# Kernel optimization log

Measured on AMD Instinct MI355X. Metric: run time of the kernel, lower is better.

## Reference

```python
import jax, jax.numpy as jnp
import numpy as np

ALPHA = 0.2  # LeakyReLU negative slope
NEG_BIG = -9e15


def setup_inputs() -> dict:
    key = jax.random.key(0)
    k1, k2, k3, k4 = jax.random.split(key, 4)
    N, F_in, F_out = 8192, 512, 256
    h = jax.random.normal(k1, (N, F_in), dtype=jnp.float32)
    adj = jax.random.randint(k2, (N, N), 0, 2, dtype=jnp.int32)
    # xavier_uniform with gain=1.414
    lim_W = 1.414 * np.sqrt(6.0 / (F_in + F_out))
    W = jax.random.uniform(k3, (F_in, F_out), jnp.float32, -lim_W, lim_W)
    lim_a = 1.414 * np.sqrt(6.0 / (2 * F_out + 1))
    a = jax.random.uniform(k4, (2 * F_out, 1), jnp.float32, -lim_a, lim_a)
    return {"h": h, "adj": adj, "W": W, "a": a}


def reference(h, adj, W, a):
    # Wh: [N, F_out]
    Wh = h @ W
    F_out = Wh.shape[1]
    # Decomposed score: e_ij = leakyrelu(a1.Wh_i + a2.Wh_j)
    f1 = Wh @ a[:F_out, 0]   # [N]
    f2 = Wh @ a[F_out:, 0]   # [N]
    e = f1[:, None] + f2[None, :]          # [N, N]
    e = jax.nn.leaky_relu(e, ALPHA)
    e = jnp.where(adj > 0, e, NEG_BIG)
    attention = jax.nn.softmax(e, axis=1)  # dropout omitted (eval mode)
    h_prime = attention @ Wh               # [N, F_out]
    return jax.nn.elu(h_prime)             # concat=True
```

## Files before the change

### kernel.cpp

```cpp
#include <hip/hip_runtime.h>
#include <hip/hip_bf16.h>
#include <cstdint>

#define NV 8192
#define FIN 512
#define FOUT 256
#define KS 4
#define ALPHA_LRELU 0.2f

using bf16x8 = __attribute__((ext_vector_type(8))) short;
using f32x4  = __attribute__((ext_vector_type(4))) float;

static __device__ __forceinline__ float b2f(ushort u) {
  union { uint32_t u32; float f; } v; v.u32 = ((uint32_t)u) << 16; return v.f;
}
static __device__ __forceinline__ ushort f2b(float f) {
  union { float f; uint32_t u; } v; v.f = f;
  uint32_t r = (v.u + 0x7fffu + ((v.u >> 16) & 1u)) >> 16;
  return (ushort)r;
}
static __device__ __forceinline__ int swz(int row, int kchunk) {
  return (row << 6) + (((kchunk ^ (row & 7)) & 7) << 3);
}
static __device__ __forceinline__ void gl_lds16(const ushort* g, ushort* l) {
  __builtin_amdgcn_global_load_lds(
      (const __attribute__((address_space(1))) uint32_t*)(uintptr_t)g,
      (__attribute__((address_space(3))) uint32_t*)(uint32_t)(uintptr_t)l,
      16, 0, 0);
}

__global__ void k_prep_h(const float* __restrict__ h, ushort* __restrict__ hB) {
  int idx = blockIdx.x * 256 + threadIdx.x;
  float4 v = ((const float4*)h)[idx];
  ushort4 o;
  o.x = f2b(v.x); o.y = f2b(v.y); o.z = f2b(v.z); o.w = f2b(v.w);
  ((ushort4*)hB)[idx] = o;
}

__global__ void k_prep_w(const float* __restrict__ W, ushort* __restrict__ WT) {
  int t = blockIdx.x * 256 + threadIdx.x;
  int n = t >> 9, k = t & 511;
  WT[(size_t)n * FIN + k] = f2b(W[(size_t)k * FOUT + n]);
}

__global__ __launch_bounds__(256, 4) void k_gemm1(
    const ushort* __restrict__ hB, const ushort* __restrict__ WT,
    ushort* __restrict__ WhT) {
  __shared__ __align__(16) ushort As[64 * 64];
  __shared__ __align__(16) ushort Ws[64 * 64];
  const int t = threadIdx.x;
  const int lane = t & 63;
  const int w = t >> 6;
  const int wm = w >> 1, wn = w & 1;
  const int i0 = blockIdx.x * 64;
  const int n0 = blockIdx.y * 64;

  f32x4 acc[2][2] = {};
  const int srow = t & 63, sseg = t >> 6;

  for (int kt = 0; kt < FIN / 64; ++kt) {
    const int k0 = kt * 64;
    const uint4* gA = (const uint4*)(hB + (size_t)(i0 + srow) * FIN + k0 + sseg * 16);
    const uint4* gB = (const uint4*)(WT + (size_t)(n0 + srow) * FIN + k0 + sseg * 16);
#pragma unroll
    for (int m = 0; m < 2; ++m) {
      uint4 va = gA[m];
      *(uint4*)&As[swz(srow, sseg * 2 + m)] = va;
      uint4 vb = gB[m];
      *(uint4*)&Ws[swz(srow, sseg * 2 + m)] = vb;
    }
    __syncthreads();
#pragma unroll
    for (int kk = 0; kk < 2; ++kk) {
      const int kc = kk * 4 + (lane >> 4);
      bf16x8 af[2], bfv[2];
#pragma unroll
      for (int fi = 0; fi < 2; ++fi)
        af[fi] = *(const bf16x8*)&As[swz(wm * 32 + fi * 16 + (lane & 15), kc)];
#pragma unroll
      for (int fj = 0; fj < 2; ++fj)
        bfv[fj] = *(const bf16x8*)&Ws[swz(wn * 32 + fj * 16 + (lane & 15), kc)];
#pragma unroll
      for (int fi = 0; fi < 2; ++fi)
#pragma unroll
        for (int fj = 0; fj < 2; ++fj)
          acc[fi][fj] = __builtin_amdgcn_mfma_f32_16x16x32_bf16(af[fi], bfv[fj], acc[fi][fj], 0, 0, 0);
    }
    __syncthreads();
  }
#pragma unroll
  for (int fi = 0; fi < 2; ++fi) {
    const int row0 = i0 + wm * 32 + fi * 16 + ((lane >> 4) << 2);
#pragma unroll
    for (int fj = 0; fj < 2; ++fj) {
      const int col = n0 + wn * 32 + fj * 16 + (lane & 15);
      ushort4 o;
      o.x = f2b(acc[fi][fj][0]); o.y = f2b(acc[fi][fj][1]);
      o.z = f2b(acc[fi][fj][2]); o.w = f2b(acc[fi][fj][3]);
      *(ushort4*)&WhT[(size_t)col * NV + row0] = o;
    }
  }
}

__global__ void k_f12(const ushort* __restrict__ WhT, const float* __restrict__ a,
                      float* __restrict__ f1, float* __restrict__ f2,
                      float* __restrict__ f2bmax) {
  __shared__ float a1s[256], a2s[256];
  __shared__ float r1[4][64], r2[4][64];
  const int tid = threadIdx.x;
  a1s[tid] = a[tid];
  a2s[tid] = a[256 + tid];
  const int ws = tid >> 6, ln = tid & 63;
  const int i = blockIdx.x * 64 + ln;
  __syncthreads();
  float s1 = 0.f, s2 = 0.f;
#pragma unroll 8
  for (int c = ws * 64; c < ws * 64 + 64; ++c) {
    float v = b2f(WhT[(size_t)c * NV + i]);
    s1 = fmaf(v, a1s[c], s1);
    s2 = fmaf(v, a2s[c], s2);
  }
  r1[ws][ln] = s1; r2[ws][ln] = s2;
  __syncthreads();
  if (ws == 0) {
    s1 = r1[0][ln] + r1[1][ln] + r1[2][ln] + r1[3][ln];
    s2 = r2[0][ln] + r2[1][ln] + r2[2][ln] + r2[3][ln];
    f1[i] = s1; f2[i] = s2;
    float m = s2;
#pragma unroll
    for (int off = 32; off > 0; off >>= 1) m = fmaxf(m, __shfl_xor(m, off));
    if (ln == 0) f2bmax[blockIdx.x] = m;
  }
}

__global__ void k_fmax(const float* __restrict__ f2bmax, float* __restrict__ mfp) {
  __shared__ float red[128];
  const int tid = threadIdx.x;
  red[tid] = f2bmax[tid];
  __syncthreads();
  for (int off = 64; off > 0; off >>= 1) {
    if (tid < off) red[tid] = fmaxf(red[tid], red[tid + off]);
    __syncthreads();
  }
  if (tid == 0) mfp[0] = red[0];
}

__global__ __launch_bounds__(512, 2) void k_gemm2(
    const int* __restrict__ adj, const ushort* __restrict__ WhT,
    const float* __restrict__ f1, const float* __restrict__ f2,
    const float* __restrict__ mfp,
    float* __restrict__ accP, float* __restrict__ Sp) {
  __shared__ __align__(16) ushort Ps[2][64 * 64];
  __shared__ __align__(16) ushort Bs[2][256 * 64];

  const int t = threadIdx.x;
  const int lane = t & 63;
  const int w = t >> 6;
  const int wm = w >> 2, wn = w & 3;
  const int bid = blockIdx.x;
  const int ks = bid & (KS - 1);
  const int rb = bid >> 2;
  const int i0 = rb * 64;
  const int jbase = ks * (NV / KS);
  const int NT = (NV / KS) / 64;

  const int pr = t >> 3, pq = t & 7;
  const float mf = mfp[0];
  const float f1r = f1[i0 + pr];
  const float e0 = f1r + mf;
  const float cr = fmaxf(e0, ALPHA_LRELU * e0);

  const int lrow = lane >> 3;
  const int lchunk = (lane & 7) ^ lrow;
  const ushort* wsrc0 = WhT + (size_t)(w * 32 + lrow) * NV + jbase + lchunk * 8;
  const int* adjp = adj + (size_t)(i0 + pr) * NV + jbase + pq * 8;
  const float* f2p = f2 + jbase + pq * 8;

  float ssum = 0.f;
  f32x4 acc[2][4] = {};
  int av[8]; float fz[8];

  auto stage_load = [&](int koff, int buf) {
#pragma unroll
    for (int q = 0; q < 4; ++q)
      gl_lds16(wsrc0 + (size_t)q * 8 * NV + koff, &Bs[buf][(w * 4 + q) * 512]);
    int4 a0 = *(const int4*)(adjp + koff);
    int4 a1 = *(const int4*)(adjp + koff + 4);
    float4 z0 = *(const float4*)(f2p + koff);
    float4 z1 = *(const float4*)(f2p + koff + 4);
    av[0] = a0.x; av[1] = a0.y; av[2] = a0.z; av[3] = a0.w;
    av[4] = a1.x; av[5] = a1.y; av[6] = a1.z; av[7] = a1.w;
    fz[0] = z0.x; fz[1] = z0.y; fz[2] = z0.z; fz[3] = z0.w;
    fz[4] = z1.x; fz[5] = z1.y; fz[6] = z1.z; fz[7] = z1.w;
  };
  auto stage_finish = [&](int buf) {
    ushort ub[8];
#pragma unroll
    for (int e = 0; e < 8; ++e) {
      float x = f1r + fz[e];
      float ee = fmaxf(x, ALPHA_LRELU * x) - cr;
      float wv = (av[e] > 0) ? __expf(ee) : 0.f;
      ub[e] = f2b(wv);
      ssum += b2f(ub[e]);
    }
    uint4 pk;
    pk.x = (uint32_t)ub[0] | ((uint32_t)ub[1] << 16);
    pk.y = (uint32_t)ub[2] | ((uint32_t)ub[3] << 16);
    pk.z = (uint32_t)ub[4] | ((uint32_t)ub[5] << 16);
    pk.w = (uint32_t)ub[6] | ((uint32_t)ub[7] << 16);
    *(uint4*)&Ps[buf][swz(pr, pq)] = pk;
  };

  stage_load(0, 0);
  stage_finish(0);
  __syncthreads();

  int cur = 0;
  for (int kt = 0; kt < NT; ++kt) {
    const bool pf = (kt + 1 < NT);
    if (pf) stage_load((kt + 1) * 64, cur ^ 1);
#pragma unroll
    for (int kk = 0; kk < 2; ++kk) {
      const int kc = kk * 4 + (lane >> 4);
      bf16x8 af[2], bfv[4];
#pragma unroll
      for (int fi = 0; fi < 2; ++fi)
        af[fi] = *(const bf16x8*)&Ps[cur][swz(wm * 32 + fi * 16 + (lane & 15), kc)];
#pragma unroll
      for (int fj = 0; fj < 4; ++fj)
        bfv[fj] = *(const bf16x8*)&Bs[cur][swz(wn * 64 + fj * 16 + (lane & 15), kc)];
#pragma unroll
      for (int fi = 0; fi < 2; ++fi)
#pragma unroll
        for (int fj = 0; fj < 4; ++fj)
          acc[fi][fj] = __builtin_amdgcn_mfma_f32_16x16x32_bf16(af[fi], bfv[fj], acc[fi][fj], 0, 0, 0);
    }
    if (pf) stage_finish(cur ^ 1);
    __syncthreads();
    cur ^= 1;
  }

  ssum += __shfl_xor(ssum, 1);
  ssum += __shfl_xor(ssum, 2);
  ssum += __shfl_xor(ssum, 4);
  if (pq == 0) Sp[(size_t)ks * NV + i0 + pr] = ssum;

  float* ab = accP + (size_t)ks * NV * FOUT;
#pragma unroll
  for (int fi = 0; fi < 2; ++fi) {
    const int ig = i0 + wm * 32 + fi * 16 + ((lane >> 4) << 2);
#pragma unroll
    for (int fj = 0; fj < 4; ++fj) {
      const int col = wn * 64 + fj * 16 + (lane & 15);
#pragma unroll
      for (int rr = 0; rr < 4; ++rr)
        ab[(size_t)(ig + rr) * FOUT + col] = acc[fi][fj][rr];
    }
  }
}

__global__ void k_combine(const float* __restrict__ accP, const float* __restrict__ Sp,
                          float* __restrict__ out) {
  const size_t NF = (size_t)NV * FOUT;
  int g = blockIdx.x * 256 + threadIdx.x;
  int i = g >> 6;
  float4 v0 = ((const float4*)accP)[g];
  float4 v1 = ((const float4*)(accP + NF))[g];
  float4 v2 = ((const float4*)(accP + 2 * NF))[g];
  float4 v3 = ((const float4*)(accP + 3 * NF))[g];
  float s = Sp[i] + Sp[NV + i] + Sp[2 * NV + i] + Sp[3 * NV + i];
  float inv = (s != 0.f) ? (1.0f / s) : 0.f;
  float xs0 = (v0.x + v1.x + v2.x + v3.x) * inv;
  float xs1 = (v0.y + v1.y + v2.y + v3.y) * inv;
  float xs2 = (v0.z + v1.z + v2.z + v3.z) * inv;
  float xs3 = (v0.w + v1.w + v2.w + v3.w) * inv;
  float4 o;
  o.x = xs0 > 0.f ? xs0 : expm1f(xs0);
  o.y = xs1 > 0.f ? xs1 : expm1f(xs1);
  o.z = xs2 > 0.f ? xs2 : expm1f(xs2);
  o.w = xs3 > 0.f ? xs3 : expm1f(xs3);
  ((float4*)out)[g] = o;
}

extern "C" void kernel_launch(void* const* d_in, const int* in_sizes, int n_in,
                              void* d_out, int out_size, void* d_ws, size_t ws_size,
                              hipStream_t stream) {
  const float* h   = (const float*)d_in[0];
  const int*   adj = (const int*)d_in[1];
  const float* W   = (const float*)d_in[2];
  const float* a   = (const float*)d_in[3];
  float* out = (float*)d_out;

  char* ws = (char*)d_ws;
  ushort* hB   = (ushort*)ws;
  ushort* WT   = (ushort*)(ws + (8ull << 20));
  ushort* WhT  = (ushort*)(ws + (8ull << 20) + (256ull << 10));
  float*  f1   = (float*)(ws + (12ull << 20) + (256ull << 10));
  float*  f2   = f1 + NV;
  float*  f2bm = f2 + NV;
  float*  mfp  = f2bm + 128;
  float*  Sp   = mfp + 64;
  float*  accP = Sp + (size_t)KS * NV;

  k_prep_h<<<(NV * FIN / 4) / 256, 256, 0, stream>>>(h, hB);
  k_prep_w<<<(FIN * FOUT) / 256, 256, 0, stream>>>(W, WT);
  k_gemm1<<<dim3(NV / 64, FOUT / 64), 256, 0, stream>>>(hB, WT, WhT);
  k_f12<<<NV / 64, 256, 0, stream>>>(WhT, a, f1, f2, f2bm);
  k_fmax<<<1, 128, 0, stream>>>(f2bm, mfp);
  k_gemm2<<<(NV / 64) * KS, 512, 0, stream>>>(adj, WhT, f1, f2, mfp, accP, Sp);
  k_combine<<<(NV * FOUT / 4) / 256, 256, 0, stream>>>(accP, Sp, out);
}
```

Before: 435.2 us.

## Fuse h conversion and f1/f2 projection into GEMM1, restructure GEMM2 pipeline

Drops the separate fp32-to-bf16 pass over h by converting inside the GEMM1 tile load. It also computes the f1/f2 attention projections in the GEMM1 epilogue, using shuffle reductions and atomics into zeroed buffers, which removes k_f12. k_fmax now reduces f2 directly with a 1024-thread block. GEMM2 gets a manually unrolled two-buffer loop that prefetches adjacency a tile further ahead, and its launch bound goes up to 4 blocks per CU. The atomics make f1/f2 summation order nondeterministic, and the higher occupancy target may force register spills.

```diff
diff --git a/kernel.cpp b/kernel.cpp
--- a/kernel.cpp
+++ b/kernel.cpp
@@ -19,6 +19,9 @@
   uint32_t r = (v.u + 0x7fffu + ((v.u >> 16) & 1u)) >> 16;
   return (ushort)r;
 }
+static __device__ __forceinline__ uint32_t pk2(float a, float b) {
+  return (uint32_t)f2b(a) | ((uint32_t)f2b(b) << 16);
+}
 static __device__ __forceinline__ int swz(int row, int kchunk) {
   return (row << 6) + (((kchunk ^ (row & 7)) & 7) << 3);
 }
@@ -29,14 +32,6 @@
       16, 0, 0);
 }
 
-__global__ void k_prep_h(const float* __restrict__ h, ushort* __restrict__ hB) {
-  int idx = blockIdx.x * 256 + threadIdx.x;
-  float4 v = ((const float4*)h)[idx];
-  ushort4 o;
-  o.x = f2b(v.x); o.y = f2b(v.y); o.z = f2b(v.z); o.w = f2b(v.w);
-  ((ushort4*)hB)[idx] = o;
-}
-
 __global__ void k_prep_w(const float* __restrict__ W, ushort* __restrict__ WT) {
   int t = blockIdx.x * 256 + threadIdx.x;
   int n = t >> 9, k = t & 511;
@@ -44,8 +39,9 @@
 }
 
 __global__ __launch_bounds__(256, 4) void k_gemm1(
-    const ushort* __restrict__ hB, const ushort* __restrict__ WT,
-    ushort* __restrict__ WhT) {
+    const float* __restrict__ h, const ushort* __restrict__ WT,
+    const float* __restrict__ a,
+    ushort* __restrict__ WhT, float* __restrict__ f1, float* __restrict__ f2) {
   __shared__ __align__(16) ushort As[64 * 64];
   __shared__ __align__(16) ushort Ws[64 * 64];
   const int t = threadIdx.x;
@@ -60,14 +56,22 @@
 
   for (int kt = 0; kt < FIN / 64; ++kt) {
     const int k0 = kt * 64;
-    const uint4* gA = (const uint4*)(hB + (size_t)(i0 + srow) * FIN + k0 + sseg * 16);
-    const uint4* gB = (const uint4*)(WT + (size_t)(n0 + srow) * FIN + k0 + sseg * 16);
-#pragma unroll
-    for (int m = 0; m < 2; ++m) {
-      uint4 va = gA[m];
-      *(uint4*)&As[swz(srow, sseg * 2 + m)] = va;
-      uint4 vb = gB[m];
-      *(uint4*)&Ws[swz(srow, sseg * 2 + m)] = vb;
+    {
+      const float4* gA = (const float4*)(h + (size_t)(i0 + srow) * FIN + k0 + sseg * 16);
+      float4 v0 = gA[0], v1 = gA[1], v2 = gA[2], v3 = gA[3];
+      uint4 c0, c1;
+      c0.x = pk2(v0.x, v0.y); c0.y = pk2(v0.z, v0.w);
+      c0.z = pk2(v1.x, v1.y); c0.w = pk2(v1.z, v1.w);
+      c1.x = pk2(v2.x, v2.y); c1.y = pk2(v2.z, v2.w);
+      c1.z = pk2(v3.x, v3.y); c1.w = pk2(v3.z, v3.w);
+      *(uint4*)&As[swz(srow, sseg * 2 + 0)] = c0;
+      *(uint4*)&As[swz(srow, sseg * 2 + 1)] = c1;
+    }
+    {
+      const uint4* gB = (const uint4*)(WT + (size_t)(n0 + srow) * FIN + k0 + sseg * 16);
+      uint4 b0 = gB[0], b1 = gB[1];
+      *(uint4*)&Ws[swz(srow, sseg * 2 + 0)] = b0;
+      *(uint4*)&Ws[swz(srow, sseg * 2 + 1)] = b1;
     }
     __syncthreads();
 #pragma unroll
@@ -88,64 +92,64 @@
     }
     __syncthreads();
   }
+
+  float p1[2][4] = {}, p2[2][4] = {};
 #pragma unroll
   for (int fi = 0; fi < 2; ++fi) {
     const int row0 = i0 + wm * 32 + fi * 16 + ((lane >> 4) << 2);
 #pragma unroll
     for (int fj = 0; fj < 2; ++fj) {
       const int col = n0 + wn * 32 + fj * 16 + (lane & 15);
+      const float a1c = a[col], a2c = a[FOUT + col];
+      ushort ov[4];
       ushort4 o;
-      o.x = f2b(acc[fi][fj][0]); o.y = f2b(acc[fi][fj][1]);
-      o.z = f2b(acc[fi][fj][2]); o.w = f2b(acc[fi][fj][3]);
+#pragma unroll
+      for (int rr = 0; rr < 4; ++rr) {
+        ov[rr] = f2b(acc[fi][fj][rr]);
+        float v = b2f(ov[rr]);
+        p1[fi][rr] = fmaf(v, a1c, p1[fi][rr]);
+        p2[fi][rr] = fmaf(v, a2c, p2[fi][rr]);
+      }
+      o.x = ov[0]; o.y = ov[1]; o.z = ov[2]; o.w = ov[3];
       *(ushort4*)&WhT[(size_t)col * NV + row0] = o;
     }
   }
-}
-
-__global__ void k_f12(const ushort* __restrict__ WhT, const float* __restrict__ a,
-                      float* __restrict__ f1, float* __restrict__ f2,
-                      float* __restrict__ f2bmax) {
-  __shared__ float a1s[256], a2s[256];
-  __shared__ float r1[4][64], r2[4][64];
+#pragma unroll
+  for (int fi = 0; fi < 2; ++fi)
+#pragma unroll
+    for (int rr = 0; rr < 4; ++rr) {
+      float s1 = p1[fi][rr], s2 = p2[fi][rr];
+#pragma unroll
+      for (int m = 1; m < 16; m <<= 1) {
+        s1 += __shfl_xor(s1, m);
+        s2 += __shfl_xor(s2, m);
+      }
+      if ((lane & 15) == 0) {
+        const int row = i0 + wm * 32 + fi * 16 + ((lane >> 4) << 2) + rr;
+        atomicAdd(&f1[row], s1);
+        atomicAdd(&f2[row], s2);
+      }
+    }
+}
+
+__global__ void k_fmax(const float* __restrict__ f2, float* __restrict__ mfp) {
+  __shared__ float red[16];
   const int tid = threadIdx.x;
-  a1s[tid] = a[tid];
-  a2s[tid] = a[256 + tid];
-  const int ws = tid >> 6, ln = tid & 63;
-  const int i = blockIdx.x * 64 + ln;
+  float m = -3e38f;
+  for (int i = tid; i < NV; i += 1024) m = fmaxf(m, f2[i]);
+#pragma unroll
+  for (int off = 32; off > 0; off >>= 1) m = fmaxf(m, __shfl_xor(m, off));
+  if ((tid & 63) == 0) red[tid >> 6] = m;
   __syncthreads();
-  float s1 = 0.f, s2 = 0.f;
-#pragma unroll 8
-  for (int c = ws * 64; c < ws * 64 + 64; ++c) {
-    float v = b2f(WhT[(size_t)c * NV + i]);
-    s1 = fmaf(v, a1s[c], s1);
-    s2 = fmaf(v, a2s[c], s2);
-  }
-  r1[ws][ln] = s1; r2[ws][ln] = s2;
-  __syncthreads();
-  if (ws == 0) {
-    s1 = r1[0][ln] + r1[1][ln] + r1[2][ln] + r1[3][ln];
-    s2 = r2[0][ln] + r2[1][ln] + r2[2][ln] + r2[3][ln];
-    f1[i] = s1; f2[i] = s2;
-    float m = s2;
-#pragma unroll
-    for (int off = 32; off > 0; off >>= 1) m = fmaxf(m, __shfl_xor(m, off));
-    if (ln == 0) f2bmax[blockIdx.x] = m;
-  }
-}
-
-__global__ void k_fmax(const float* __restrict__ f2bmax, float* __restrict__ mfp) {
-  __shared__ float red[128];
-  const int tid = threadIdx.x;
-  red[tid] = f2bmax[tid];
-  __syncthreads();
-  for (int off = 64; off > 0; off >>= 1) {
-    if (tid < off) red[tid] = fmaxf(red[tid], red[tid + off]);
-    __syncthreads();
-  }
-  if (tid == 0) mfp[0] = red[0];
-}
-
-__global__ __launch_bounds__(512, 2) void k_gemm2(
+  if (tid < 64) {
+    float v = (tid < 16) ? red[tid] : -3e38f;
+#pragma unroll
+    for (int off = 8; off > 0; off >>= 1) v = fmaxf(v, __shfl_xor(v, off));
+    if (tid == 0) mfp[0] = v;
+  }
+}
+
+__global__ __launch_bounds__(512, 4) void k_gemm2(
     const int* __restrict__ adj, const ushort* __restrict__ WhT,
     const float* __restrict__ f1, const float* __restrict__ f2,
     const float* __restrict__ mfp,
@@ -178,22 +182,28 @@
 
   float ssum = 0.f;
   f32x4 acc[2][4] = {};
-  int av[8]; float fz[8];
-
-  auto stage_load = [&](int koff, int buf) {
+  int avA[8], avB[8];
+  float fz[8];
+
+  auto adjload = [&](int tile, int (&av)[8]) {
+    int4 a0 = *(const int4*)(adjp + tile * 64);
+    int4 a1 = *(const int4*)(adjp + tile * 64 + 4);
+    av[0] = a0.x; av[1] = a0.y; av[2] = a0.z; av[3] = a0.w;
+    av[4] = a1.x; av[5] = a1.y; av[6] = a1.z; av[7] = a1.w;
+  };
+  auto fzload = [&](int tile) {
+    float4 z0 = *(const float4*)(f2p + tile * 64);
+    float4 z1 = *(const float4*)(f2p + tile * 64 + 4);
+    fz[0] = z0.x; fz[1] = z0.y; fz[2] = z0.z; fz[3] = z0.w;
+    fz[4] = z1.x; fz[5] = z1.y; fz[6] = z1.z; fz[7] = z1.w;
+  };
+  auto glB = [&](int tile, int buf) {
+    const int koff = tile * 64;
 #pragma unroll
     for (int q = 0; q < 4; ++q)
       gl_lds16(wsrc0 + (size_t)q * 8 * NV + koff, &Bs[buf][(w * 4 + q) * 512]);
-    int4 a0 = *(const int4*)(adjp + koff);
-    int4 a1 = *(const int4*)(adjp + koff + 4);
-    float4 z0 = *(const float4*)(f2p + koff);
-    float4 z1 = *(const float4*)(f2p + koff + 4);
-    av[0] = a0.x; av[1] = a0.y; av[2] = a0.z; av[3] = a0.w;
-    av[4] = a1.x; av[5] = a1.y; av[6] = a1.z; av[7] = a1.w;
-    fz[0] = z0.x; fz[1] = z0.y; fz[2] = z0.z; fz[3] = z0.w;
-    fz[4] = z1.x; fz[5] = z1.y; fz[6] = z1.z; fz[7] = z1.w;
-  };
-  auto stage_finish = [&](int buf) {
+  };
+  auto finish = [&](const int (&av)[8], int buf) {
     ushort ub[8];
 #pragma unroll
     for (int e = 0; e < 8; ++e) {
@@ -210,34 +220,47 @@
     pk.w = (uint32_t)ub[6] | ((uint32_t)ub[7] << 16);
     *(uint4*)&Ps[buf][swz(pr, pq)] = pk;
   };
-
-  stage_load(0, 0);
-  stage_finish(0);
-  __syncthreads();
-
-  int cur = 0;
-  for (int kt = 0; kt < NT; ++kt) {
-    const bool pf = (kt + 1 < NT);
-    if (pf) stage_load((kt + 1) * 64, cur ^ 1);
+  auto mfma_step = [&](int buf) {
 #pragma unroll
     for (int kk = 0; kk < 2; ++kk) {
       const int kc = kk * 4 + (lane >> 4);
       bf16x8 af[2], bfv[4];
 #pragma unroll
       for (int fi = 0; fi < 2; ++fi)
-        af[fi] = *(const bf16x8*)&Ps[cur][swz(wm * 32 + fi * 16 + (lane & 15), kc)];
+        af[fi] = *(const bf16x8*)&Ps[buf][swz(wm * 32 + fi * 16 + (lane & 15), kc)];
 #pragma unroll
       for (int fj = 0; fj < 4; ++fj)
-        bfv[fj] = *(const bf16x8*)&Bs[cur][swz(wn * 64 + fj * 16 + (lane & 15), kc)];
+        bfv[fj] = *(const bf16x8*)&Bs[buf][swz(wn * 64 + fj * 16 + (lane & 15), kc)];
 #pragma unroll
       for (int fi = 0; fi < 2; ++fi)
 #pragma unroll
         for (int fj = 0; fj < 4; ++fj)
           acc[fi][fj] = __builtin_amdgcn_mfma_f32_16x16x32_bf16(af[fi], bfv[fj], acc[fi][fj], 0, 0, 0);
     }
-    if (pf) stage_finish(cur ^ 1);
+  };
+
+  adjload(0, avA);
+  adjload(1, avB);
+  glB(0, 0);
+  fzload(0);
+  finish(avA, 0);
+  __syncthreads();
+
+  for (int kt = 0; kt < NT; kt += 2) {
+    glB(kt + 1, 1);
+    if (kt + 2 < NT) adjload(kt + 2, avA);
+    fzload(kt + 1);
+    mfma_step(0);
+    finish(avB, 1);
     __syncthreads();
-    cur ^= 1;
+    if (kt + 2 < NT) {
+      glB(kt + 2, 0);
+      if (kt + 3 < NT) adjload(kt + 3, avB);
+      fzload(kt + 2);
+    }
+    mfma_step(1);
+    if (kt + 2 < NT) finish(avA, 0);
+    __syncthreads();
   }
 
   ssum += __shfl_xor(ssum, 1);
@@ -292,21 +315,18 @@
   float* out = (float*)d_out;
 
   char* ws = (char*)d_ws;
-  ushort* hB   = (ushort*)ws;
-  ushort* WT   = (ushort*)(ws + (8ull << 20));
-  ushort* WhT  = (ushort*)(ws + (8ull << 20) + (256ull << 10));
-  float*  f1   = (float*)(ws + (12ull << 20) + (256ull << 10));
+  ushort* WT   = (ushort*)ws;
+  ushort* WhT  = (ushort*)(ws + (256ull << 10));
+  float*  f1   = (float*)(ws + (256ull << 10) + (4ull << 20));
   float*  f2   = f1 + NV;
-  float*  f2bm = f2 + NV;
-  float*  mfp  = f2bm + 128;
+  float*  mfp  = f2 + NV;
   float*  Sp   = mfp + 64;
   float*  accP = Sp + (size_t)KS * NV;
 
-  k_prep_h<<<(NV * FIN / 4) / 256, 256, 0, stream>>>(h, hB);
+  hipMemsetAsync(f1, 0, 2 * NV * sizeof(float), stream);
   k_prep_w<<<(FIN * FOUT) / 256, 256, 0, stream>>>(W, WT);
-  k_gemm1<<<dim3(NV / 64, FOUT / 64), 256, 0, stream>>>(hB, WT, WhT);
-  k_f12<<<NV / 64, 256, 0, stream>>>(WhT, a, f1, f2, f2bm);
-  k_fmax<<<1, 128, 0, stream>>>(f2bm, mfp);
+  k_gemm1<<<dim3(NV / 64, FOUT / 64), 256, 0, stream>>>(h, WT, a, WhT, f1, f2);
+  k_fmax<<<1, 1024, 0, stream>>>(f2, mfp);
   k_gemm2<<<(NV / 64) * KS, 512, 0, stream>>>(adj, WhT, f1, f2, mfp, accP, Sp);
   k_combine<<<(NV * FOUT / 4) / 256, 256, 0, stream>>>(accP, Sp, out);
 }
```

New measurement: 430.6 us. About the same (-1.0%).
